# Performance work log

Hardware: AMD Instinct MI355X
Metric: run time of the kernel (lower is better)

## Reference

```python
import jax, jax.numpy as jnp
import numpy as np

NEG_SLOPE = 0.2  # PyG GATConv default negative_slope


def _gat_conv(h, src, dst, N, W, a_src, a_dst, b, heads):
    """PyG GATConv (eval mode, self-loops already in src/dst).
    h: [N, F_in], W: [F_in, heads*C], a_src/a_dst: [heads, C], b: [heads*C]."""
    C = W.shape[1] // heads
    hl = (h @ W).reshape(N, heads, C)                      # [N,H,C]
    al_s = jnp.einsum('nhc,hc->nh', hl, a_src)             # [N,H]
    al_d = jnp.einsum('nhc,hc->nh', hl, a_dst)             # [N,H]
    e = jax.nn.leaky_relu(al_s[src] + al_d[dst], NEG_SLOPE)  # [E,H]
    # segment softmax over incoming edges of each destination node
    m = jax.ops.segment_max(e, dst, num_segments=N)        # [N,H]
    ex = jnp.exp(e - m[dst])
    s = jax.ops.segment_sum(ex, dst, num_segments=N)
    alpha = ex / (s[dst] + 1e-16)                          # [E,H]
    out = jax.ops.segment_sum(hl[src] * alpha[:, :, None], dst, num_segments=N)
    return out.reshape(N, heads * C) + b


def setup_inputs() -> dict:
    key = jax.random.key(0)
    ks = jax.random.split(key, 16)
    N, E, D = 30000, 240000, 64
    NUM_ENT, NUM_REL, NUM_DRUGS = 100000, 64, 200
    sc = 0.1
    return {
        'x': jax.random.randint(ks[0], (N,), 0, NUM_ENT),
        'edge_index': jax.random.randint(ks[1], (2, E), 0, N),
        'edge_type': jax.random.randint(ks[2], (N,), 0, NUM_REL),
        'ent_emb': jax.random.normal(ks[3], (NUM_ENT, D), jnp.float32) * sc,
        'rel_emb': jax.random.normal(ks[4], (NUM_REL, D), jnp.float32) * sc,
        'W1': jax.random.normal(ks[5], (2 * D, 8 * D), jnp.float32) * sc,
        'att1_src': jax.random.normal(ks[6], (8, D), jnp.float32) * sc,
        'att1_dst': jax.random.normal(ks[7], (8, D), jnp.float32) * sc,
        'b1': jax.random.normal(ks[8], (8 * D,), jnp.float32) * sc,
        'W2': jax.random.normal(ks[9], (9 * D, D), jnp.float32) * sc,
        'att2_src': jax.random.normal(ks[10], (1, D), jnp.float32) * sc,
        'att2_dst': jax.random.normal(ks[11], (1, D), jnp.float32) * sc,
        'b2': jax.random.normal(ks[12], (D,), jnp.float32) * sc,
        'fc_w': jax.random.normal(ks[13], (D, NUM_DRUGS), jnp.float32) * sc,
        'fc_b': jax.random.normal(ks[14], (NUM_DRUGS,), jnp.float32) * sc,
    }


def reference(x, edge_index, edge_type, ent_emb, rel_emb, W1, att1_src, att1_dst, b1,
              W2, att2_src, att2_dst, b2, fc_w, fc_b):
    N = x.shape[0]
    loop = jnp.arange(N)
    src = jnp.concatenate([edge_index[0], loop])  # GATConv add_self_loops=True
    dst = jnp.concatenate([edge_index[1], loop])
    ent = ent_emb[x]                               # [N,D]
    rel = rel_emb[edge_type]                       # [N,D]
    h = jnp.concatenate([ent, rel], axis=-1)       # [N,2D]  (dropout is identity in eval)
    h = jax.nn.elu(_gat_conv(h, src, dst, N, W1, att1_src, att1_dst, b1, heads=8))  # [N,8D]
    h = jnp.concatenate([h, ent], axis=-1)         # [N,9D]
    h = jax.nn.elu(_gat_conv(h, src, dst, N, W2, att2_src, att2_dst, b2, heads=1))  # [N,D]
    g = jnp.mean(h, axis=0, keepdims=True)         # [1,D]
    return g @ fc_w + fc_b                         # [1,num_drugs]
```

## Files before the change

kernel.cpp:

```cpp
#include <hip/hip_runtime.h>
#include <math.h>

#define NEG_SLOPE 0.2f

typedef __attribute__((ext_vector_type(8))) short short8;
typedef __attribute__((ext_vector_type(4))) float f32x4;
typedef __attribute__((ext_vector_type(2))) float f32x2;

__device__ __forceinline__ float lrelu(float v) { return v > 0.f ? v : NEG_SLOPE * v; }
__device__ __forceinline__ float elu(float v) { return v > 0.f ? v : (__expf(v) - 1.f); }
__device__ __forceinline__ unsigned short f2b(float f) {
    unsigned u = __float_as_uint(f);
    return (unsigned short)((u + 0x7FFFu + ((u >> 16) & 1u)) >> 16);
}
__device__ __forceinline__ float blo(unsigned v) { return __uint_as_float(v << 16); }
__device__ __forceinline__ float bhi(unsigned v) { return __uint_as_float(v & 0xFFFF0000u); }
__device__ __forceinline__ unsigned packb(float a, float b) {
    return ((unsigned)f2b(b) << 16) | (unsigned)f2b(a);
}
__device__ __forceinline__ unsigned short pack8(float a, float b) {
    return (unsigned short)(__builtin_amdgcn_cvt_pk_fp8_f32(a, b, 0, false) & 0xFFFF);
}
__device__ __forceinline__ f32x2 unpack8(unsigned v) {
    return __builtin_amdgcn_cvt_pk_f32_fp8((int)v, false);
}
__device__ __forceinline__ int sw(int r, int o) { return (o ^ (r & 7)) << 3; }

__global__ __launch_bounds__(256) void init_k(int* __restrict__ zbase, int zwords,
                                              const float* __restrict__ W1,
                                              const float* __restrict__ W2,
                                              const float* __restrict__ a1s,
                                              const float* __restrict__ a1d,
                                              unsigned short* __restrict__ wsb,
                                              unsigned short* __restrict__ W1t,
                                              unsigned short* __restrict__ W2t) {
    int t = blockIdx.x * blockDim.x + threadIdx.x;
    int stride = gridDim.x * blockDim.x;
    for (int i = t; i < zwords; i += stride) zbase[i] = 0;
    for (int i = t; i < 2048; i += stride) {
        int hh = i >> 7, k = i & 127, h = hh & 7;
        const float* aw = (hh < 8) ? a1s : a1d;
        const float* wr = W1 + (size_t)k * 512 + h * 64;
        float s_ = 0.f;
#pragma unroll 16
        for (int c = 0; c < 64; c++) s_ += wr[c] * aw[h * 64 + c];
        wsb[i] = f2b(s_);
    }
    for (int i = t; i < 512 * 128; i += stride) {
        int n = i >> 7, kk = i & 127;
        W1t[i] = f2b(W1[(size_t)kk * 512 + n]);
    }
    for (int i = t; i < 64 * 576; i += stride) {
        int n = i / 576, k = i % 576;
        W2t[i] = f2b(W2[(size_t)k * 64 + n]);
    }
}

__global__ void prep_k(const int* __restrict__ x, const int* __restrict__ et,
                       const int* __restrict__ ei,
                       const float* __restrict__ ent_emb, const float* __restrict__ rel_emb,
                       unsigned* __restrict__ h1b2, unsigned short* __restrict__ h1q,
                       int* __restrict__ deg, int N, int E) {
    int t = blockIdx.x * blockDim.x + threadIdx.x;
    if (t < N * 64) {
        int n = t >> 6, j = t & 63;
        float v0, v1;
        if (j < 32) {
            const float* e = ent_emb + (size_t)x[n] * 64 + 2 * j;
            v0 = e[0]; v1 = e[1];
        } else {
            const float* r = rel_emb + (size_t)et[n] * 64 + 2 * (j - 32);
            v0 = r[0]; v1 = r[1];
        }
        h1b2[t] = packb(v0, v1);
        h1q[t] = pack8(v0, v1);
    }
    if (t < E + N) {
        int dst = t < E ? ei[E + t] : t - E;
        atomicAdd(&deg[dst], 1);
    }
}

__global__ __launch_bounds__(256) void attn1_k(const unsigned short* __restrict__ A,
                                               const unsigned short* __restrict__ Bt,
                                               float* __restrict__ als, float* __restrict__ ald,
                                               int M) {
    __shared__ __align__(16) unsigned short As[128 * 128];
    __shared__ __align__(16) unsigned short Bs[16 * 128];
    int tid = threadIdx.x;
    int m0 = blockIdx.x * 128;
    for (int c = tid; c < 2048; c += 256) {
        int r = c >> 4, o = c & 15;
        int gr = m0 + r;
        uint4 v = make_uint4(0u, 0u, 0u, 0u);
        if (gr < M) v = *(const uint4*)(A + (size_t)gr * 128 + o * 8);
        *(uint4*)(As + r * 128 + sw(r, o)) = v;
    }
    if (tid < 256) {
        int r = tid >> 4, o = tid & 15;
        uint4 v = *(const uint4*)(Bt + (size_t)r * 128 + o * 8);
        *(uint4*)(Bs + r * 128 + sw(r, o)) = v;
    }
    __syncthreads();
    int w = tid >> 6, lane = tid & 63;
    int wr = w * 32;
    int m16 = lane & 15, quad = lane >> 4;
    f32x4 acc[2] = {};
#pragma unroll
    for (int kk = 0; kk < 128; kk += 32) {
        int ob = (kk >> 3) + quad;
        short8 b = *(const short8*)(Bs + m16 * 128 + sw(m16, ob));
#pragma unroll
        for (int i = 0; i < 2; i++) {
            int r = wr + i * 16 + m16;
            short8 a = *(const short8*)(As + r * 128 + sw(r, ob));
            acc[i] = __builtin_amdgcn_mfma_f32_16x16x32_bf16(a, b, acc[i], 0, 0, 0);
        }
    }
#pragma unroll
    for (int i = 0; i < 2; i++)
#pragma unroll
        for (int reg = 0; reg < 4; reg++) {
            int row = m0 + wr + i * 16 + quad * 4 + reg;
            if (row < M) {
                if (m16 < 8) als[row * 8 + m16] = acc[i][reg];
                else         ald[row * 8 + (m16 - 8)] = acc[i][reg];
            }
        }
}

__global__ __launch_bounds__(256) void scan_k(const int* __restrict__ deg,
                                              int* __restrict__ offs,
                                              int* __restrict__ bstate,
                                              int N, int Etot, int NB) {
    __shared__ int s[256];
    __shared__ int sbase;
    int b = blockIdx.x, t = threadIdx.x;
    int i = b * 256 + t;
    int v = (i < N) ? deg[i] : 0;
    s[t] = v;
    __syncthreads();
    for (int off = 1; off < 256; off <<= 1) {
        int tmp = (t >= off) ? s[t - off] : 0;
        __syncthreads();
        s[t] += tmp;
        __syncthreads();
    }
    int total = s[255];
    if (t == 0) {
        if (b == 0) {
            atomicExch(&bstate[0], (total << 2) | 2);
            sbase = 0;
        } else {
            atomicExch(&bstate[b], (total << 2) | 1);
            int run = 0;
            for (int p = b - 1; p >= 0;) {
                int stv;
                do { stv = atomicAdd(&bstate[p], 0); } while ((stv & 3) == 0);
                run += (stv >> 2);
                if ((stv & 3) == 2) break;
                p--;
            }
            atomicExch(&bstate[b], ((run + total) << 2) | 2);
            sbase = run;
        }
    }
    __syncthreads();
    if (i < N) offs[i] = sbase + s[t] - v;
    if (b == NB - 1 && t == 0) offs[N] = Etot;
}

__global__ void fill_k(const int* __restrict__ ei, int E, int N,
                       const int* __restrict__ offs, int* __restrict__ cursor,
                       int* __restrict__ csr) {
    int e = blockIdx.x * blockDim.x + threadIdx.x;
    if (e >= E + N) return;
    int src = e < E ? ei[e] : e - E;
    int dst = e < E ? ei[E + e] : e - E;
    int pos = offs[dst] + atomicAdd(&cursor[dst], 1);
    csr[pos] = src;
}

__global__ __launch_bounds__(64) void aggG_k(const unsigned short* __restrict__ h1q,
                                             const unsigned* __restrict__ h1b2,
                                             const float* __restrict__ als1,
                                             const float* __restrict__ ald1,
                                             const int* __restrict__ offs,
                                             const int* __restrict__ csr,
                                             unsigned* __restrict__ Gu,
                                             unsigned* __restrict__ h2u, int N) {
    int n = blockIdx.x;
    int t = threadIdx.x;
    int hh = t & 7;
    float dl = ald1[n * 8 + hh];
    int p0 = offs[n], p1 = offs[n + 1];
    float a0[8] = {}, a1[8] = {};
    float ssacc = 0.f;
    for (int p = p0; p < p1; p++) {
        int src = csr[p];
        float xv = __expf(lrelu(als1[src * 8 + hh] + dl));
        ssacc += xv;
        unsigned hv = h1q[(size_t)src * 64 + t];
        f32x2 f = unpack8(hv);
        float ev[8];
#pragma unroll
        for (int h = 0; h < 8; h++) ev[h] = __shfl(xv, h, 64);
#pragma unroll
        for (int h = 0; h < 8; h++) {
            a0[h] += ev[h] * f.x;
            a1[h] += ev[h] * f.y;
        }
    }
#pragma unroll
    for (int h = 0; h < 8; h++) {
        float iv = 1.f / (__shfl(ssacc, h, 64) + 1e-16f);
        Gu[(size_t)n * 512 + h * 64 + t] = packb(a0[h] * iv, a1[h] * iv);
    }
    if (t < 32)
        h2u[(size_t)n * 288 + 256 + t] = h1b2[(size_t)n * 64 + t];
}

__global__ __launch_bounds__(256) void gemmG_k(const unsigned short* __restrict__ Gb,
                                               const unsigned short* __restrict__ W1t,
                                               const float* __restrict__ b1,
                                               unsigned short* __restrict__ h2, int M) {
    __shared__ __align__(16) unsigned short As[128 * 128];
    __shared__ __align__(16) unsigned short Bs[64 * 128];
    int tid = threadIdx.x;
    int m0 = blockIdx.x * 128, h = blockIdx.y;
    for (int c = tid; c < 2048; c += 256) {
        int r = c >> 4, o = c & 15;
        int gr = m0 + r;
        uint4 v = make_uint4(0u, 0u, 0u, 0u);
        if (gr < M) v = *(const uint4*)(Gb + (size_t)gr * 1024 + h * 128 + o * 8);
        *(uint4*)(As + r * 128 + sw(r, o)) = v;
    }
    for (int c = tid; c < 1024; c += 256) {
        int r = c >> 4, o = c & 15;
        uint4 v = *(const uint4*)(W1t + (size_t)(h * 64 + r) * 128 + o * 8);
        *(uint4*)(Bs + r * 128 + sw(r, o)) = v;
    }
    __syncthreads();
    int w = tid >> 6, lane = tid & 63;
    int wr = w * 32;
    int m16 = lane & 15, quad = lane >> 4;
    f32x4 acc[2][4] = {};
#pragma unroll
    for (int kk = 0; kk < 128; kk += 32) {
        int ob = (kk >> 3) + quad;
        short8 b[4];
#pragma unroll
        for (int j = 0; j < 4; j++) {
            int r = j * 16 + m16;
            b[j] = *(const short8*)(Bs + r * 128 + sw(r, ob));
        }
#pragma unroll
        for (int i = 0; i < 2; i++) {
            int r = wr + i * 16 + m16;
            short8 a = *(const short8*)(As + r * 128 + sw(r, ob));
#pragma unroll
            for (int j = 0; j < 4; j++)
                acc[i][j] = __builtin_amdgcn_mfma_f32_16x16x32_bf16(a, b[j], acc[i][j], 0, 0, 0);
        }
    }
#pragma unroll
    for (int i = 0; i < 2; i++)
#pragma unroll
        for (int j = 0; j < 4; j++)
#pragma unroll
            for (int reg = 0; reg < 4; reg++) {
                int row = m0 + wr + i * 16 + quad * 4 + reg;
                int col = h * 64 + j * 16 + m16;
                if (row < M) h2[(size_t)row * 576 + col] = f2b(elu(acc[i][j][reg] + b1[col]));
            }
}

__global__ __launch_bounds__(256) void gemm2_k(const unsigned short* __restrict__ A,
                                               const unsigned short* __restrict__ Bt,
                                               const float* __restrict__ a2s,
                                               const float* __restrict__ a2d,
                                               unsigned char* __restrict__ hl2q,
                                               float* __restrict__ als2,
                                               float* __restrict__ ald2, int M) {
    __shared__ __align__(16) unsigned short As[64 * 64];
    __shared__ __align__(16) unsigned short Bs[64 * 64];
    int tid = threadIdx.x;
    int m0 = blockIdx.x * 64;
    int w = tid >> 6, lane = tid & 63;
    int m16 = lane & 15, quad = lane >> 4;
    f32x4 acc[4] = {};
    for (int k0 = 0; k0 < 576; k0 += 64) {
        __syncthreads();
        for (int c = tid; c < 512; c += 256) {
            int r = c >> 3, o = c & 7;
            int gr = m0 + r;
            uint4 v = make_uint4(0u, 0u, 0u, 0u);
            if (gr < M) v = *(const uint4*)(A + (size_t)gr * 576 + k0 + o * 8);
            *(uint4*)(As + r * 64 + sw(r, o)) = v;
        }
        for (int c = tid; c < 512; c += 256) {
            int r = c >> 3, o = c & 7;
            uint4 v = *(const uint4*)(Bt + (size_t)r * 576 + k0 + o * 8);
            *(uint4*)(Bs + r * 64 + sw(r, o)) = v;
        }
        __syncthreads();
#pragma unroll
        for (int kk = 0; kk < 64; kk += 32) {
            int ob = (kk >> 3) + quad;
            int r = w * 16 + m16;
            short8 a = *(const short8*)(As + r * 64 + sw(r, ob));
#pragma unroll
            for (int j = 0; j < 4; j++) {
                int rb = j * 16 + m16;
                short8 b = *(const short8*)(Bs + rb * 64 + sw(rb, ob));
                acc[j] = __builtin_amdgcn_mfma_f32_16x16x32_bf16(a, b, acc[j], 0, 0, 0);
            }
        }
    }
#pragma unroll
    for (int j = 0; j < 4; j++)
#pragma unroll
        for (int reg = 0; reg < 4; reg++) {
            int row = m0 + w * 16 + quad * 4 + reg;
            int col = j * 16 + m16;
            if (row < M)
                hl2q[(size_t)row * 64 + col] =
                    (unsigned char)(__builtin_amdgcn_cvt_pk_fp8_f32(acc[j][reg], 0.f, 0, false) & 0xFF);
        }
    float sa[4] = {}, sd[4] = {};
#pragma unroll
    for (int j = 0; j < 4; j++) {
        int col = j * 16 + m16;
        float as_ = a2s[col], ad_ = a2d[col];
#pragma unroll
        for (int reg = 0; reg < 4; reg++) {
            sa[reg] += acc[j][reg] * as_;
            sd[reg] += acc[j][reg] * ad_;
        }
    }
#pragma unroll
    for (int m = 1; m < 16; m <<= 1)
#pragma unroll
        for (int reg = 0; reg < 4; reg++) {
            sa[reg] += __shfl_xor(sa[reg], m, 64);
            sd[reg] += __shfl_xor(sd[reg], m, 64);
        }
    if (m16 == 0)
#pragma unroll
        for (int reg = 0; reg < 4; reg++) {
            int row = m0 + w * 16 + quad * 4 + reg;
            if (row < M) { als2[row] = sa[reg]; ald2[row] = sd[reg]; }
        }
}

__global__ __launch_bounds__(256) void agg2_k(const unsigned short* __restrict__ hl2q16,
                                              const float* __restrict__ als2,
                                              const float* __restrict__ ald2,
                                              const float* __restrict__ b2,
                                              const int* __restrict__ offs,
                                              const int* __restrict__ csr,
                                              float* __restrict__ gpart, int N) {
    __shared__ float red[512];
    int slot = threadIdx.x >> 5, l = threadIdx.x & 31;
    int n = blockIdx.x * 8 + slot;
    float v0 = 0.f, v1 = 0.f;
    if (n < N) {
        float dl = ald2[n];
        int p0 = offs[n], p1 = offs[n + 1];
        float a0 = 0.f, a1 = 0.f, ssum = 0.f;
        for (int p = p0; p < p1; p++) {
            int src = csr[p];
            float xv = __expf(lrelu(als2[src] + dl));
            ssum += xv;
            unsigned v = hl2q16[(size_t)src * 32 + l];
            f32x2 f = unpack8(v);
            a0 += xv * f.x;
            a1 += xv * f.y;
        }
        float inv = 1.f / (ssum + 1e-16f);
        v0 = elu(a0 * inv + b2[2 * l]);
        v1 = elu(a1 * inv + b2[2 * l + 1]);
    }
    red[slot * 64 + 2 * l] = v0;
    red[slot * 64 + 2 * l + 1] = v1;
    __syncthreads();
    if (threadIdx.x < 64) {
        float s = 0.f;
#pragma unroll
        for (int ss = 0; ss < 8; ss++) s += red[ss * 64 + threadIdx.x];
        gpart[(size_t)blockIdx.x * 64 + threadIdx.x] = s;
    }
}

__global__ __launch_bounds__(256) void colredfinal_k(const float* __restrict__ gpart,
                                                     float* __restrict__ gsum,
                                                     int* __restrict__ done,
                                                     const float* __restrict__ fcw,
                                                     const float* __restrict__ fcb,
                                                     float* __restrict__ out,
                                                     int NBL, int N, int NCB) {
    __shared__ float red[256];
    __shared__ int isLast;
    int t = threadIdx.x;
    int c = t & 63, rg = t >> 6;
    int bend = blockIdx.x * 256 + 256; if (bend > NBL) bend = NBL;
    float acc = 0.f;
    for (int b = blockIdx.x * 256 + rg; b < bend; b += 4)
        acc += gpart[(size_t)b * 64 + c];
    red[t] = acc;
    __syncthreads();
    if (t < 64) atomicAdd(&gsum[c], red[c] + red[c + 64] + red[c + 128] + red[c + 192]);
    __threadfence();
    if (t == 0) {
        int old = atomicAdd(done, 1);
        isLast = (old == NCB - 1) ? 1 : 0;
    }
    __syncthreads();
    if (isLast) {
        __shared__ float g[64];
        if (t < 64) g[t] = atomicAdd(&gsum[t], 0.f) / (float)N;
        __syncthreads();
        if (t < 200) {
            float a = fcb[t];
#pragma unroll
            for (int cc = 0; cc < 64; cc++) a += g[cc] * fcw[cc * 200 + t];
            out[t] = a;
        }
    }
}

extern "C" void kernel_launch(void* const* d_in, const int* in_sizes, int n_in,
                              void* d_out, int out_size, void* d_ws, size_t ws_size,
                              hipStream_t stream) {
    const int* x = (const int*)d_in[0];
    const int* ei = (const int*)d_in[1];
    const int* et = (const int*)d_in[2];
    const float* ent_emb = (const float*)d_in[3];
    const float* rel_emb = (const float*)d_in[4];
    const float* W1 = (const float*)d_in[5];
    const float* a1s = (const float*)d_in[6];
    const float* a1d = (const float*)d_in[7];
    const float* b1 = (const float*)d_in[8];
    const float* W2 = (const float*)d_in[9];
    const float* a2s = (const float*)d_in[10];
    const float* a2d = (const float*)d_in[11];
    const float* b2 = (const float*)d_in[12];
    const float* fcw = (const float*)d_in[13];
    const float* fcb = (const float*)d_in[14];
    float* out = (float*)d_out;

    int N = in_sizes[0];
    int E = in_sizes[1] / 2;
    int Etot = E + N;
    int NB = (N + 255) / 256;
    int NBL = (N + 7) / 8;
    int NCB = (NBL + 255) / 256;

    char* p = (char*)d_ws;
    auto alloc = [&](size_t bytes) -> char* {
        char* r = p;
        p += (bytes + 255) & ~(size_t)255;
        return r;
    };
    unsigned* h1b2 = (unsigned*)alloc((size_t)N * 64 * 4);
    unsigned short* h1q = (unsigned short*)alloc((size_t)N * 64 * 2);
    unsigned short* wsb = (unsigned short*)alloc(2048 * 2);
    unsigned short* W1t = (unsigned short*)alloc((size_t)512 * 128 * 2);
    unsigned short* W2t = (unsigned short*)alloc((size_t)64 * 576 * 2);
    float* als1 = (float*)alloc((size_t)N * 8 * 4);
    float* ald1 = (float*)alloc((size_t)N * 8 * 4);
    unsigned* Gu = (unsigned*)alloc((size_t)N * 512 * 4);
    unsigned short* h2  = (unsigned short*)alloc((size_t)N * 576 * 2);
    unsigned char* hl2q = (unsigned char*)alloc((size_t)N * 64);
    float* als2 = (float*)alloc((size_t)N * 4);
    float* ald2 = (float*)alloc((size_t)N * 4);
    float* gpart = (float*)alloc((size_t)NBL * 64 * 4);
    int* offs   = (int*)alloc((size_t)(N + 1) * 4);
    int* csr    = (int*)alloc((size_t)Etot * 4);
    char* z0 = p;
    int* deg    = (int*)alloc((size_t)N * 4);
    int* cursor = (int*)alloc((size_t)N * 4);
    float* gsum = (float*)alloc(64 * 4);
    int* done   = (int*)alloc(4);
    int* bstate = (int*)alloc((size_t)NB * 4);
    size_t zwords = (size_t)(p - z0) / 4;

    int tb = 256;
    init_k<<<256, tb, 0, stream>>>((int*)z0, (int)zwords, W1, W2, a1s, a1d, wsb, W1t, W2t);
    prep_k<<<(N * 64 + tb - 1) / tb, tb, 0, stream>>>(x, et, ei, ent_emb, rel_emb,
                                                      h1b2, h1q, deg, N, E);
    attn1_k<<<(N + 127) / 128, 256, 0, stream>>>((const unsigned short*)h1b2, wsb, als1, ald1, N);
    scan_k<<<NB, 256, 0, stream>>>(deg, offs, bstate, N, Etot, NB);
    fill_k<<<(Etot + tb - 1) / tb, tb, 0, stream>>>(ei, E, N, offs, cursor, csr);
    aggG_k<<<N, 64, 0, stream>>>(h1q, h1b2, als1, ald1, offs, csr, Gu, (unsigned*)h2, N);
    gemmG_k<<<dim3((N + 127) / 128, 8), 256, 0, stream>>>((const unsigned short*)Gu, W1t, b1, h2, N);
    gemm2_k<<<(N + 63) / 64, 256, 0, stream>>>(h2, W2t, a2s, a2d, hl2q, als2, ald2, N);
    agg2_k<<<NBL, 256, 0, stream>>>((const unsigned short*)hl2q, als2, ald2, b2, offs, csr, gpart, N);
    colredfinal_k<<<NCB, 256, 0, stream>>>(gpart, gsum, done, fcw, fcb, out, NBL, N, NCB);
}
```

Before: 272.5 us.

## Store aggregated layer-1 features as scaled FP8 and unroll edge loops by two

The per-node aggregated G matrix is now written as FP8, pre-scaled by 8 to keep values in FP8 range, instead of bf16. This halves the intermediate traffic between the aggregation and the GEMM. The GEMM unpacks FP8 to bf16 while loading into shared memory and divides the scale back out in the epilogue. Aggregation now packs four nodes per 256-thread block, and both aggregation kernels process two edges per iteration to overlap gathers. The FP8 storage adds quantization error to an intermediate result, and the extra unpacking adds ALU work inside the GEMM load.

New measurement: 270.5 us. About the same (-0.7%).

```diff
diff --git a/kernel.cpp b/kernel.cpp
--- a/kernel.cpp
+++ b/kernel.cpp
@@ -23,6 +23,12 @@
 }
 __device__ __forceinline__ f32x2 unpack8(unsigned v) {
     return __builtin_amdgcn_cvt_pk_f32_fp8((int)v, false);
+}
+__device__ __forceinline__ f32x2 unpack8hi(unsigned v) {
+    return __builtin_amdgcn_cvt_pk_f32_fp8((int)v, true);
+}
+__device__ __forceinline__ unsigned bpack_trunc(f32x2 f) {
+    return (__float_as_uint(f.y) & 0xFFFF0000u) | (__float_as_uint(f.x) >> 16);
 }
 __device__ __forceinline__ int sw(int r, int o) { return (o ^ (r & 7)) << 3; }
 
@@ -181,46 +187,65 @@
     csr[pos] = src;
 }
 
-__global__ __launch_bounds__(64) void aggG_k(const unsigned short* __restrict__ h1q,
-                                             const unsigned* __restrict__ h1b2,
-                                             const float* __restrict__ als1,
-                                             const float* __restrict__ ald1,
-                                             const int* __restrict__ offs,
-                                             const int* __restrict__ csr,
-                                             unsigned* __restrict__ Gu,
-                                             unsigned* __restrict__ h2u, int N) {
-    int n = blockIdx.x;
-    int t = threadIdx.x;
+__global__ __launch_bounds__(256) void aggG_k(const unsigned short* __restrict__ h1q,
+                                              const unsigned* __restrict__ h1b2,
+                                              const float* __restrict__ als1,
+                                              const float* __restrict__ ald1,
+                                              const int* __restrict__ offs,
+                                              const int* __restrict__ csr,
+                                              unsigned short* __restrict__ Gq,
+                                              unsigned* __restrict__ h2u, int N) {
+    int wv = threadIdx.x >> 6;
+    int t = threadIdx.x & 63;
+    int n = blockIdx.x * 4 + wv;
+    if (n >= N) return;
     int hh = t & 7;
     float dl = ald1[n * 8 + hh];
     int p0 = offs[n], p1 = offs[n + 1];
     float a0[8] = {}, a1[8] = {};
     float ssacc = 0.f;
-    for (int p = p0; p < p1; p++) {
-        int src = csr[p];
-        float xv = __expf(lrelu(als1[src * 8 + hh] + dl));
-        ssacc += xv;
-        unsigned hv = h1q[(size_t)src * 64 + t];
-        f32x2 f = unpack8(hv);
-        float ev[8];
-#pragma unroll
-        for (int h = 0; h < 8; h++) ev[h] = __shfl(xv, h, 64);
+    int p = p0;
+    for (; p + 1 < p1; p += 2) {
+        int sA = csr[p], sB = csr[p + 1];
+        float lA = als1[sA * 8 + hh];
+        float lB = als1[sB * 8 + hh];
+        unsigned hA = h1q[(size_t)sA * 64 + t];
+        unsigned hB = h1q[(size_t)sB * 64 + t];
+        float xA = __expf(lrelu(lA + dl));
+        float xB = __expf(lrelu(lB + dl));
+        ssacc += xA + xB;
+        f32x2 fA = unpack8(hA);
+        f32x2 fB = unpack8(hB);
+        float evA[8], evB[8];
+#pragma unroll
+        for (int h = 0; h < 8; h++) { evA[h] = __shfl(xA, h, 64); evB[h] = __shfl(xB, h, 64); }
 #pragma unroll
         for (int h = 0; h < 8; h++) {
-            a0[h] += ev[h] * f.x;
-            a1[h] += ev[h] * f.y;
-        }
+            a0[h] += evA[h] * fA.x + evB[h] * fB.x;
+            a1[h] += evA[h] * fA.y + evB[h] * fB.y;
+        }
+    }
+    if (p < p1) {
+        int sA = csr[p];
+        float xA = __expf(lrelu(als1[sA * 8 + hh] + dl));
+        ssacc += xA;
+        f32x2 fA = unpack8(h1q[(size_t)sA * 64 + t]);
+        float evA[8];
+#pragma unroll
+        for (int h = 0; h < 8; h++) evA[h] = __shfl(xA, h, 64);
+#pragma unroll
+        for (int h = 0; h < 8; h++) { a0[h] += evA[h] * fA.x; a1[h] += evA[h] * fA.y; }
     }
 #pragma unroll
     for (int h = 0; h < 8; h++) {
-        float iv = 1.f / (__shfl(ssacc, h, 64) + 1e-16f);
-        Gu[(size_t)n * 512 + h * 64 + t] = packb(a0[h] * iv, a1[h] * iv);
+        float iv = 8.f / (__shfl(ssacc, h, 64) + 1e-16f);
+        Gq[(size_t)(n * 8 + h) * 64 + t] = pack8(a0[h] * iv, a1[h] * iv);
     }
     if (t < 32)
         h2u[(size_t)n * 288 + 256 + t] = h1b2[(size_t)n * 64 + t];
 }
 
-__global__ __launch_bounds__(256) void gemmG_k(const unsigned short* __restrict__ Gb,
+__global__ __launch_bounds__(256) void gemmG_k(const unsigned char* __restrict__ Gq8,
                                                const unsigned short* __restrict__ W1t,
                                                const float* __restrict__ b1,
                                                unsigned short* __restrict__ h2, int M) {
@@ -228,12 +253,18 @@
     __shared__ __align__(16) unsigned short Bs[64 * 128];
     int tid = threadIdx.x;
     int m0 = blockIdx.x * 128, h = blockIdx.y;
-    for (int c = tid; c < 2048; c += 256) {
-        int r = c >> 4, o = c & 15;
+    for (int c = tid; c < 1024; c += 256) {
+        int r = c >> 3, o = c & 7;
         int gr = m0 + r;
         uint4 v = make_uint4(0u, 0u, 0u, 0u);
-        if (gr < M) v = *(const uint4*)(Gb + (size_t)gr * 1024 + h * 128 + o * 8);
-        *(uint4*)(As + r * 128 + sw(r, o)) = v;
+        if (gr < M) v = *(const uint4*)(Gq8 + ((size_t)gr * 8 + h) * 128 + o * 16);
+        uint4 w0, w1;
+        w0.x = bpack_trunc(unpack8(v.x));   w0.y = bpack_trunc(unpack8hi(v.x));
+        w0.z = bpack_trunc(unpack8(v.y));   w0.w = bpack_trunc(unpack8hi(v.y));
+        w1.x = bpack_trunc(unpack8(v.z));   w1.y = bpack_trunc(unpack8hi(v.z));
+        w1.z = bpack_trunc(unpack8(v.w));   w1.w = bpack_trunc(unpack8hi(v.w));
+        *(uint4*)(As + r * 128 + sw(r, 2 * o)) = w0;
+        *(uint4*)(As + r * 128 + sw(r, 2 * o + 1)) = w1;
     }
     for (int c = tid; c < 1024; c += 256) {
         int r = c >> 4, o = c & 15;
@@ -271,7 +302,8 @@
             for (int reg = 0; reg < 4; reg++) {
                 int row = m0 + wr + i * 16 + quad * 4 + reg;
                 int col = h * 64 + j * 16 + m16;
-                if (row < M) h2[(size_t)row * 576 + col] = f2b(elu(acc[i][j][reg] + b1[col]));
+                if (row < M)
+                    h2[(size_t)row * 576 + col] = f2b(elu(acc[i][j][reg] * 0.125f + b1[col]));
             }
 }
 
@@ -368,14 +400,26 @@
         float dl = ald2[n];
         int p0 = offs[n], p1 = offs[n + 1];
         float a0 = 0.f, a1 = 0.f, ssum = 0.f;
-        for (int p = p0; p < p1; p++) {
-            int src = csr[p];
-            float xv = __expf(lrelu(als2[src] + dl));
-            ssum += xv;
-            unsigned v = hl2q16[(size_t)src * 32 + l];
-            f32x2 f = unpack8(v);
-            a0 += xv * f.x;
-            a1 += xv * f.y;
+        int p = p0;
+        for (; p + 1 < p1; p += 2) {
+            int sA = csr[p], sB = csr[p + 1];
+            float lA = als2[sA], lB = als2[sB];
+            unsigned hA = hl2q16[(size_t)sA * 32 + l];
+            unsigned hB = hl2q16[(size_t)sB * 32 + l];
+            float xA = __expf(lrelu(lA + dl));
+            float xB = __expf(lrelu(lB + dl));
+            ssum += xA + xB;
+            f32x2 fA = unpack8(hA), fB = unpack8(hB);
+            a0 += xA * fA.x + xB * fB.x;
+            a1 += xA * fA.y + xB * fB.y;
+        }
+        if (p < p1) {
+            int sA = csr[p];
+            float xA = __expf(lrelu(als2[sA] + dl));
+            ssum += xA;
+            f32x2 fA = unpack8(hl2q16[(size_t)sA * 32 + l]);
+            a0 += xA * fA.x;
+            a1 += xA * fA.y;
         }
         float inv = 1.f / (ssum + 1e-16f);
         v0 = elu(a0 * inv + b2[2 * l]);
@@ -469,7 +513,7 @@
     unsigned short* W2t = (unsigned short*)alloc((size_t)64 * 576 * 2);
     float* als1 = (float*)alloc((size_t)N * 8 * 4);
     float* ald1 = (float*)alloc((size_t)N * 8 * 4);
-    unsigned* Gu = (unsigned*)alloc((size_t)N * 512 * 4);
+    unsigned short* Gq = (unsigned short*)alloc((size_t)N * 512 * 2);
     unsigned short* h2  = (unsigned short*)alloc((size_t)N * 576 * 2);
     unsigned char* hl2q = (unsigned char*)alloc((size_t)N * 64);
     float* als2 = (float*)alloc((size_t)N * 4);
@@ -492,8 +536,8 @@
     attn1_k<<<(N + 127) / 128, 256, 0, stream>>>((const unsigned short*)h1b2, wsb, als1, ald1, N);
     scan_k<<<NB, 256, 0, stream>>>(deg, offs, bstate, N, Etot, NB);
     fill_k<<<(Etot + tb - 1) / tb, tb, 0, stream>>>(ei, E, N, offs, cursor, csr);
-    aggG_k<<<N, 64, 0, stream>>>(h1q, h1b2, als1, ald1, offs, csr, Gu, (unsigned*)h2, N);
-    gemmG_k<<<dim3((N + 127) / 128, 8), 256, 0, stream>>>((const unsigned short*)Gu, W1t, b1, h2, N);
+    aggG_k<<<(N + 3) / 4, 256, 0, stream>>>(h1q, h1b2, als1, ald1, offs, csr, Gq, (unsigned*)h2, N);
+    gemmG_k<<<dim3((N + 127) / 128, 8), 256, 0, stream>>>((const unsigned char*)Gq, W1t, b1, h2, N);
     gemm2_k<<<(N + 63) / 64, 256, 0, stream>>>(h2, W2t, a2s, a2d, hl2q, als2, ald2, N);
     agg2_k<<<NBL, 256, 0, stream>>>((const unsigned short*)hl2q, als2, ald2, b2, offs, csr, gpart, N);
     colredfinal_k<<<NCB, 256, 0, stream>>>(gpart, gsum, done, fcw, fcb, out, NBL, N, NCB);
```
